# Optimization experiments

Measured on AMD Instinct MI355X. Metric: run time of the kernel, lower is better.

Reference implementation:

```python
import jax, jax.numpy as jnp
import numpy as np

B, T, C, H, W = 2, 4, 3, 96, 96
HF, L = 128, 6
TC = T * C
EPS = 1e-5


def swish(x):
    return x * jax.nn.sigmoid(x)


def _build_edges(h, w):
    # self-loops + 8-neighbor grid edges, exactly as image_to_graph
    edges = [np.stack([np.arange(h * w)] * 2)]
    nx0, ny0 = np.meshgrid(np.arange(w), np.arange(h), indexing='ij')
    for dx, dy in [(-1, -1), (0, -1), (1, -1), (-1, 0), (1, 0), (-1, 1), (0, 1), (1, 1)]:
        nx, ny = nx0 + dx, ny0 + dy
        src = ny * w + nx
        dst = (ny - dy) * w + (nx - dx)
        ok = (nx >= 0) & (nx < w) & (0 <= ny) & (ny < h)
        edges.append(np.stack([src[ok], dst[ok]]))
    return np.concatenate(edges, axis=1)


def setup_inputs() -> dict:
    key = jax.random.key(0)
    ks = iter(jax.random.split(key, 40))

    def lin(fi, fo):
        return jax.random.normal(next(ks), (fi, fo), jnp.float32) / np.sqrt(fi).astype(np.float32)

    x = jax.random.normal(next(ks), (B, T, C, H, W), jnp.float32)
    ei = _build_edges(H, W)
    px, py = np.meshgrid(np.arange(W), np.arange(H), indexing='ij')
    pos = np.stack([px.flatten(), py.flatten()], 1).astype(np.float32) / (H - 1)
    return dict(
        x=x,
        edge_src=jnp.asarray(ei[0], jnp.int32),
        edge_dst=jnp.asarray(ei[1], jnp.int32),
        pos=jnp.asarray(pos),
        emb_w1=lin(TC + 2, HF), emb_b1=jnp.zeros((HF,), jnp.float32),
        emb_w2=lin(HF, HF), emb_b2=jnp.zeros((HF,), jnp.float32),
        msg_w1=jnp.stack([lin(2 * HF + TC + 1, HF) for _ in range(L)]),
        msg_b1=jnp.zeros((L, HF), jnp.float32),
        msg_w2=jnp.stack([lin(HF, HF) for _ in range(L)]),
        msg_b2=jnp.zeros((L, HF), jnp.float32),
        upd_w1=jnp.stack([lin(2 * HF, HF) for _ in range(L)]),
        upd_b1=jnp.zeros((L, HF), jnp.float32),
        upd_w2=jnp.stack([lin(HF, HF) for _ in range(L)]),
        upd_b2=jnp.zeros((L, HF), jnp.float32),
        out_w1=lin(HF, HF), out_b1=jnp.zeros((HF,), jnp.float32),
        out_w2=lin(HF, C), out_b2=jnp.zeros((C,), jnp.float32),
    )


def _forward(x, emb_w1, emb_b1, emb_w2, emb_b2, msg_w1, msg_b1, msg_w2, msg_b2,
             upd_w1, upd_b1, upd_w2, upd_b2, out_w1, out_b1, out_w2, out_b2,
             edge_src, edge_dst, pos):
    b, t, c, h, w = x.shape
    n = h * w
    u = x.reshape(b, t * c, n).transpose(0, 2, 1)                       # [B,N,TC]
    node_in = jnp.concatenate([u, jnp.broadcast_to(pos, (b, n, 2))], -1)
    hf = swish(swish(node_in @ emb_w1 + emb_b1) @ emb_w2 + emb_b2)      # [B,N,HF]
    dist = jnp.linalg.norm(pos[edge_dst] - pos[edge_src], axis=1, keepdims=True)  # [E,1]
    dist_b = jnp.broadcast_to(dist, (b,) + dist.shape)
    deg = jnp.zeros((n,), x.dtype).at[edge_dst].add(1.0)                # >=1 (self loops)
    for l in range(msg_w1.shape[0]):
        m_in = jnp.concatenate([hf[:, edge_dst], hf[:, edge_src],
                                u[:, edge_dst] - u[:, edge_src], dist_b], -1)
        m = swish(swish(m_in @ msg_w1[l] + msg_b1[l]) @ msg_w2[l] + msg_b2[l])
        agg = jnp.zeros(hf.shape, hf.dtype).at[:, edge_dst].add(m) / deg[None, :, None]
        upd = swish(swish(jnp.concatenate([hf, agg], -1) @ upd_w1[l] + upd_b1[l])
                    @ upd_w2[l] + upd_b2[l])
        hf = hf + upd                                                    # residual (in==out)
        mu = hf.mean(axis=1, keepdims=True)                              # InstanceNorm per graph
        var = hf.var(axis=1, keepdims=True)
        hf = (hf - mu) * jax.lax.rsqrt(var + EPS)
    hg = hf.reshape(b, h, w, -1)
    diff = (swish(hg @ out_w1 + out_b1) @ out_w2 + out_b2).transpose(0, 3, 1, 2)
    return (x[:, -1] + diff)[:, None]                                    # [B,1,C,H,W]


def reference(x, edge_src, edge_dst, pos, emb_w1, emb_b1, emb_w2, emb_b2,
              msg_w1, msg_b1, msg_w2, msg_b2, upd_w1, upd_b1, upd_w2, upd_b2,
              out_w1, out_b1, out_w2, out_b2):
    return _forward(x, emb_w1, emb_b1, emb_w2, emb_b2, msg_w1, msg_b1, msg_w2, msg_b2,
                    upd_w1, upd_b1, upd_w2, upd_b2, out_w1, out_b1, out_w2, out_b2,
                    edge_src, edge_dst, pos)
```

## Files before the change

### kernel.cpp

```cpp
#include <hip/hip_runtime.h>
#include <math.h>

#define HF 128
#define NB 9216
#define BB 2
#define MROWS (BB*NB)
#define GH 96
#define GW 96
#define LAYERS 6

typedef __attribute__((ext_vector_type(8))) short bf16x8;
typedef __attribute__((ext_vector_type(4))) float f32x4;

#define MFMA16(a, b, c) __builtin_amdgcn_mfma_f32_16x16x32_bf16(a, b, c, 0, 0, 0)

__device__ __forceinline__ float swishf(float x) {
    return __fdividef(x, 1.0f + __expf(-x));
}

__device__ __forceinline__ unsigned short f2b(float f) {
    unsigned u = __float_as_uint(f);
    unsigned r = (u + 0x7fffu + ((u >> 16) & 1u)) >> 16;
    return (unsigned short)r;
}
__device__ __forceinline__ float b2f(unsigned short u) {
    return __uint_as_float((unsigned)u << 16);
}

__device__ __forceinline__ bf16x8 norm_frag(const float* __restrict__ hp,
                                            const float* __restrict__ mus,
                                            const float* __restrict__ rss, int k0) {
    float4 h0 = *(const float4*)hp;
    float4 h1 = *(const float4*)(hp + 4);
    float4 m0 = *(const float4*)&mus[k0];
    float4 m1 = *(const float4*)&mus[k0 + 4];
    float4 r0 = *(const float4*)&rss[k0];
    float4 r1 = *(const float4*)&rss[k0 + 4];
    union { bf16x8 v; unsigned u[4]; } az;
    float a0 = (h0.x - m0.x) * r0.x, a1 = (h0.y - m0.y) * r0.y;
    az.u[0] = (unsigned)f2b(a0) | ((unsigned)f2b(a1) << 16);
    float a2 = (h0.z - m0.z) * r0.z, a3 = (h0.w - m0.w) * r0.w;
    az.u[1] = (unsigned)f2b(a2) | ((unsigned)f2b(a3) << 16);
    float a4 = (h1.x - m1.x) * r1.x, a5 = (h1.y - m1.y) * r1.y;
    az.u[2] = (unsigned)f2b(a4) | ((unsigned)f2b(a5) << 16);
    float a6 = (h1.z - m1.z) * r1.z, a7 = (h1.w - m1.w) * r1.w;
    az.u[3] = (unsigned)f2b(a6) | ((unsigned)f2b(a7) << 16);
    return az.v;
}

__global__ void k_prep(const float* __restrict__ embw2, const float* __restrict__ outw1,
                       const float* __restrict__ msgw1, const float* __restrict__ msgw2,
                       const float* __restrict__ updw1, const float* __restrict__ updw2,
                       unsigned short* __restrict__ wT) {
    int s = blockIdx.x;
    const float* src;
    if (s == 0) src = embw2;
    else if (s == 1) src = outw1;
    else {
        int l = (s - 2) / 6, r = (s - 2) % 6;
        if (r == 0)      src = msgw1 + (size_t)l * 269 * HF;
        else if (r == 1) src = msgw1 + (size_t)l * 269 * HF + HF * HF;
        else if (r == 2) src = msgw2 + (size_t)l * HF * HF;
        else if (r == 3) src = updw1 + (size_t)l * 256 * HF;
        else if (r == 4) src = updw1 + (size_t)l * 256 * HF + HF * HF;
        else             src = updw2 + (size_t)l * HF * HF;
    }
    __shared__ float tile[128][133];
    int t = threadIdx.x;
#pragma unroll
    for (int i = 0; i < 64; ++i) {
        int id = i * 256 + t;
        tile[id >> 7][id & 127] = src[id];
    }
    __syncthreads();
    unsigned short* o = wT + (size_t)s * 16384;
#pragma unroll
    for (int i = 0; i < 64; ++i) {
        int id = i * 256 + t;
        int col = id >> 7, k = id & 127;
        o[id] = f2b(tile[k][col]);
    }
}

__global__ void k_build(const float* __restrict__ x, const float* __restrict__ pos,
                        float* __restrict__ nodein, float* __restrict__ musig) {
    int t = threadIdx.x;
    int idx = blockIdx.x * 256 + t;
    if (blockIdx.x == 0 && t < 256) {
        musig[t] = 0.0f;
        musig[256 + t] = 1.0f;
    }
    if (idx >= MROWS) return;
    int b = idx / NB, n = idx - b * NB;
    float* o = nodein + (size_t)idx * 16;
    const float* xb = x + (size_t)b * 12 * NB + n;
#pragma unroll
    for (int k = 0; k < 12; ++k) o[k] = xb[(size_t)k * NB];
    o[12] = pos[2 * n];
    o[13] = pos[2 * n + 1];
    o[14] = 0.0f; o[15] = 0.0f;
}

__global__ __launch_bounds__(256, 4)
void k_emb(const float* __restrict__ nodein, const float* __restrict__ w1,
           const float* __restrict__ b1, const unsigned short* __restrict__ wT2,
           const float* __restrict__ b2, float* __restrict__ hf) {
    __shared__ float xs[16][14];
    __shared__ char t1s[4096];
    int t = threadIdx.x;
    int rt = blockIdx.x * 16;
    if (t < 224) {
        int r = t / 14, k = t - r * 14;
        xs[r][k] = nodein[(size_t)(rt + r) * 16 + k];
    }
    __syncthreads();
    {
        int f = t & 127, rblk = t >> 7;
        float wreg[14];
#pragma unroll
        for (int k = 0; k < 14; ++k) wreg[k] = w1[k * HF + f];
        float bv = b1[f];
#pragma unroll
        for (int i = 0; i < 8; ++i) {
            int row = rblk * 8 + i;
            float acc = bv;
#pragma unroll
            for (int k = 0; k < 14; ++k) acc = fmaf(xs[row][k], wreg[k], acc);
            int addr = (row * 256 + f * 2) ^ ((row & 7) << 4);
            *(unsigned short*)(t1s + addr) = f2b(swishf(acc));
        }
    }
    __syncthreads();
    int wave = t >> 6, lane = t & 63, lr = lane & 15, lg = lane >> 4;
    int fb = wave * 32;
    f32x4 acc[2];
    acc[0] = (f32x4)0.0f; acc[1] = (f32x4)0.0f;
#pragma unroll
    for (int kc = 0; kc < 4; ++kc) {
        int k0 = kc * 32 + lg * 8;
        bf16x8 a = *(const bf16x8*)(t1s + ((lr * 256 + k0 * 2) ^ ((lr & 7) << 4)));
#pragma unroll
        for (int j = 0; j < 2; ++j) {
            bf16x8 b = *(const bf16x8*)(wT2 + (size_t)(fb + j * 16 + lr) * HF + k0);
            acc[j] = MFMA16(a, b, acc[j]);
        }
    }
#pragma unroll
    for (int j = 0; j < 2; ++j) {
        int f = fb + j * 16 + lr;
        float bv = b2[f];
#pragma unroll
        for (int r = 0; r < 4; ++r) {
            size_t o = (size_t)(rt + lg * 4 + r) * HF + f;
            hf[o] = swishf(acc[j][r] + bv);
        }
    }
}

__global__ __launch_bounds__(256, 4)
void k_as(const float* __restrict__ hf, const float* __restrict__ musig,
          const unsigned short* __restrict__ wA, const unsigned short* __restrict__ wB,
          const float* __restrict__ nodein, const float* __restrict__ w1u,
          unsigned short* __restrict__ A, unsigned short* __restrict__ S) {
    __shared__ float w1s[12][128];
    __shared__ float mus[128], rss[128];
    int t = threadIdx.x, wave = t >> 6, lane = t & 63, lr = lane & 15, lg = lane >> 4;
    int rt = blockIdx.x * 16;
    int b = blockIdx.x / (NB / 16);
    int fb = wave * 32;
    for (int i = t; i < 12 * 128; i += 256) w1s[i >> 7][i & 127] = w1u[i];
    if (t < 128) { mus[t] = musig[b * 128 + t]; rss[t] = musig[256 + b * 128 + t]; }
    __syncthreads();
    f32x4 accA[2], accS[2];
    accA[0] = (f32x4)0.0f; accA[1] = (f32x4)0.0f;
    accS[0] = (f32x4)0.0f; accS[1] = (f32x4)0.0f;
#pragma unroll
    for (int kc = 0; kc < 4; ++kc) {
        int k0 = kc * 32 + lg * 8;
        bf16x8 a = norm_frag(hf + (size_t)(rt + lr) * HF + k0, mus, rss, k0);
#pragma unroll
        for (int j = 0; j < 2; ++j) {
            bf16x8 bA = *(const bf16x8*)(wA + (size_t)(fb + j * 16 + lr) * HF + k0);
            accA[j] = MFMA16(a, bA, accA[j]);
            bf16x8 bS = *(const bf16x8*)(wB + (size_t)(fb + j * 16 + lr) * HF + k0);
            accS[j] = MFMA16(a, bS, accS[j]);
        }
    }
    float ni[4][12];
#pragma unroll
    for (int r = 0; r < 4; ++r) {
        const float4* np = (const float4*)(nodein + (size_t)(rt + lg * 4 + r) * 16);
        float4 v0 = np[0], v1 = np[1], v2 = np[2];
        ni[r][0] = v0.x; ni[r][1] = v0.y; ni[r][2] = v0.z; ni[r][3] = v0.w;
        ni[r][4] = v1.x; ni[r][5] = v1.y; ni[r][6] = v1.z; ni[r][7] = v1.w;
        ni[r][8] = v2.x; ni[r][9] = v2.y; ni[r][10] = v2.z; ni[r][11] = v2.w;
    }
#pragma unroll
    for (int j = 0; j < 2; ++j) {
        int f = fb + j * 16 + lr;
        float au[4] = {0.f, 0.f, 0.f, 0.f};
#pragma unroll
        for (int k = 0; k < 12; ++k) {
            float wv = w1s[k][f];
#pragma unroll
            for (int r = 0; r < 4; ++r) au[r] = fmaf(ni[r][k], wv, au[r]);
        }
#pragma unroll
        for (int r = 0; r < 4; ++r) {
            size_t o = (size_t)(rt + lg * 4 + r) * HF + f;
            A[o] = f2b(accA[j][r] + au[r]);
            S[o] = f2b(accS[j][r] - au[r]);
        }
    }
}

__global__ __launch_bounds__(256, 4)
void k_agg(const unsigned short* __restrict__ Ab, const unsigned short* __restrict__ Sb,
           const unsigned short* __restrict__ wT2, const float* __restrict__ b2,
           const float* __restrict__ b1, const float* __restrict__ w1d,
           unsigned short* __restrict__ aggb) {
    __shared__ float dsb[3][128];
    __shared__ char exb[9 * 4096];
    int t = threadIdx.x, kq = t >> 6, lane = t & 63, lr = lane & 15, lg = lane >> 4;
    int bx = blockIdx.x;
    int b = bx / (NB / 16), tile = bx % (NB / 16);
    int rt = tile * 16;
    int fb = kq * 32;
    size_t bN = (size_t)b * NB;
    int R = rt / GW, C0 = rt % GW;

    if (t < 128) {
        float bb = b1[t], wd = w1d[t];
        dsb[0][t] = bb;
        dsb[1][t] = fmaf(1.0f / 95.0f, wd, bb);
        dsb[2][t] = fmaf(1.4142135623730951f / 95.0f, wd, bb);
    }
    bf16x8 w2f[2][4];
#pragma unroll
    for (int j = 0; j < 2; ++j)
#pragma unroll
        for (int kc = 0; kc < 4; ++kc)
            w2f[j][kc] = *(const bf16x8*)(wT2 + (size_t)(fb + j * 16 + lr) * HF
                                          + kc * 32 + lg * 8);
    int rowA = rt + lr;
    float Af[8];
    {
        bf16x8 av = *(const bf16x8*)(Ab + (bN + rowA) * HF + kq * 32 + lg * 8);
#pragma unroll
        for (int e = 0; e < 8; ++e) Af[e] = b2f((unsigned short)av[e]);
    }
    float b2r[2] = { b2[fb + lr], b2[fb + 16 + lr] };
    int lofs = lane * 16;
    __syncthreads();

    bf16x8 sv;
    {
        int src = min(max(rowA - 97, 0), NB - 1);
        sv = *(const bf16x8*)(Sb + (bN + src) * HF + kq * 32 + lg * 8);
    }
#pragma unroll
    for (int off = 0; off < 9; ++off) {
        int dr = off / 3 - 1, dc = off % 3 - 1;
        int dd = dr * dr + dc * dc;
        bf16x8 cur = sv;
        if (off < 8) {
            int no = off + 1;
            int dnn = (no / 3 - 1) * GW + (no % 3 - 1);
            int src = min(max(rowA + dnn, 0), NB - 1);
            sv = *(const bf16x8*)(Sb + (bN + src) * HF + kq * 32 + lg * 8);
        }
        const float* dp = &dsb[dd][kq * 32 + lg * 8];
        union { bf16x8 v; unsigned u[4]; } az;
#pragma unroll
        for (int q = 0; q < 4; ++q) {
            float zl = swishf(Af[2 * q]     + b2f((unsigned short)cur[2 * q])     + dp[2 * q]);
            float zh = swishf(Af[2 * q + 1] + b2f((unsigned short)cur[2 * q + 1]) + dp[2 * q + 1]);
            az.u[q] = (unsigned)f2b(zl) | ((unsigned)f2b(zh) << 16);
        }
        *(bf16x8*)(exb + off * 4096 + kq * 1024 + lofs) = az.v;
    }
    __syncthreads();

    f32x4 agg2[2];
    agg2[0] = (f32x4)0.0f; agg2[1] = (f32x4)0.0f;
#pragma unroll
    for (int off = 0; off < 9; ++off) {
        int dr = off / 3 - 1, dc = off % 3 - 1;
        f32x4 acc[2];
        acc[0] = (f32x4)0.0f; acc[1] = (f32x4)0.0f;
#pragma unroll
        for (int kc = 0; kc < 4; ++kc) {
            bf16x8 a = *(const bf16x8*)(exb + off * 4096 + kc * 1024 + lofs);
            acc[0] = MFMA16(a, w2f[0][kc], acc[0]);
            acc[1] = MFMA16(a, w2f[1][kc], acc[1]);
        }
        bool rOK = (unsigned)(R + dr) < (unsigned)GH;
#pragma unroll
        for (int j = 0; j < 2; ++j)
#pragma unroll
            for (int r = 0; r < 4; ++r) {
                int C = C0 + lg * 4 + r;
                if (rOK && (unsigned)(C + dc) < (unsigned)GW)
                    agg2[j][r] += swishf(acc[j][r] + b2r[j]);
            }
    }
    float nr = 1.0f + (R > 0) + (R < GH - 1);
#pragma unroll
    for (int j = 0; j < 2; ++j)
#pragma unroll
        for (int r = 0; r < 4; ++r) {
            int n = rt + lg * 4 + r;
            int C = C0 + lg * 4 + r;
            float nc = 1.0f + (C > 0) + (C < GW - 1);
            aggb[(bN + n) * HF + fb + j * 16 + lr] =
                f2b(__fdividef(agg2[j][r], nr * nc));
        }
}

__global__ __launch_bounds__(256, 4)
void k_upd(float* __restrict__ hf, const float* __restrict__ musig,
           const unsigned short* __restrict__ aggb,
           const unsigned short* __restrict__ w1a, const unsigned short* __restrict__ w1b,
           const unsigned short* __restrict__ w2, const float* __restrict__ b1v,
           const float* __restrict__ b2v, float* __restrict__ partial) {
    __shared__ char t1s[4096];
    __shared__ float mus[128], rss[128];
    int t = threadIdx.x, wave = t >> 6, lane = t & 63, lr = lane & 15, lg = lane >> 4;
    int rt = blockIdx.x * 16;
    int b = blockIdx.x / (NB / 16);
    int fb = wave * 32;
    if (t < 128) { mus[t] = musig[b * 128 + t]; rss[t] = musig[256 + b * 128 + t]; }
    __syncthreads();
    f32x4 acc[2];
    acc[0] = (f32x4)0.0f; acc[1] = (f32x4)0.0f;
#pragma unroll
    for (int kc = 0; kc < 4; ++kc) {
        int k0 = kc * 32 + lg * 8;
        bf16x8 a1 = norm_frag(hf + (size_t)(rt + lr) * HF + k0, mus, rss, k0);
        bf16x8 a2 = *(const bf16x8*)(aggb + (size_t)(rt + lr) * HF + k0);
#pragma unroll
        for (int j = 0; j < 2; ++j) {
            bf16x8 bA = *(const bf16x8*)(w1a + (size_t)(fb + j * 16 + lr) * HF + k0);
            acc[j] = MFMA16(a1, bA, acc[j]);
            bf16x8 bB = *(const bf16x8*)(w1b + (size_t)(fb + j * 16 + lr) * HF + k0);
            acc[j] = MFMA16(a2, bB, acc[j]);
        }
    }
#pragma unroll
    for (int j = 0; j < 2; ++j) {
        int col = fb + j * 16 + lr;
        float bv = b1v[col];
#pragma unroll
        for (int r = 0; r < 4; ++r) {
            int row = lg * 4 + r;
            int addr = (row * 256 + col * 2) ^ ((row & 7) << 4);
            *(unsigned short*)(t1s + addr) = f2b(swishf(acc[j][r] + bv));
        }
    }
    __syncthreads();
    f32x4 acc2[2];
    acc2[0] = (f32x4)0.0f; acc2[1] = (f32x4)0.0f;
#pragma unroll
    for (int kc = 0; kc < 4; ++kc) {
        int k0 = kc * 32 + lg * 8;
        bf16x8 a = *(const bf16x8*)(t1s + ((lr * 256 + k0 * 2) ^ ((lr & 7) << 4)));
#pragma unroll
        for (int j = 0; j < 2; ++j) {
            bf16x8 b = *(const bf16x8*)(w2 + (size_t)(fb + j * 16 + lr) * HF + k0);
            acc2[j] = MFMA16(a, b, acc2[j]);
        }
    }
#pragma unroll
    for (int j = 0; j < 2; ++j) {
        int f = fb + j * 16 + lr;
        float bv = b2v[f];
        float mu = mus[f], rs = rss[f];
        float s1 = 0.f, s2 = 0.f;
#pragma unroll
        for (int r = 0; r < 4; ++r) {
            size_t o = (size_t)(rt + lg * 4 + r) * HF + f;
            float v = swishf(acc2[j][r] + bv) + (hf[o] - mu) * rs;
            hf[o] = v;
            s1 += v; s2 += v * v;
        }
        s1 += __shfl_xor(s1, 16); s1 += __shfl_xor(s1, 32);
        s2 += __shfl_xor(s2, 16); s2 += __shfl_xor(s2, 32);
        if (lg == 0) {
            float* p = partial + ((size_t)blockIdx.x * HF + f) * 2;
            p[0] = s1; p[1] = s2;
        }
    }
}

__global__ void k_stats(const float* __restrict__ partial, float* __restrict__ musig) {
    __shared__ float ss[256], qq[256];
    int bx = blockIdx.x;
    int b = bx >> 7, f = bx & 127;
    int t = threadIdx.x;
    float s = 0.f, q = 0.f;
    for (int i = t; i < 576; i += 256) {
        const float* p = partial + (((size_t)(b * 576 + i)) * HF + f) * 2;
        s += p[0]; q += p[1];
    }
    ss[t] = s; qq[t] = q;
    __syncthreads();
    for (int st = 128; st > 0; st >>= 1) {
        if (t < st) { ss[t] += ss[t + st]; qq[t] += qq[t + st]; }
        __syncthreads();
    }
    if (t == 0) {
        float mu = ss[0] * (1.0f / NB);
        float var = qq[0] * (1.0f / NB) - mu * mu;
        musig[bx] = mu;
        musig[256 + bx] = rsqrtf(var + 1e-5f);
    }
}

__global__ __launch_bounds__(256, 4)
void k_out(const float* __restrict__ hf, const float* __restrict__ musig,
           const unsigned short* __restrict__ wT1, const float* __restrict__ b1,
           const float* __restrict__ w2, const float* __restrict__ b2,
           const float* __restrict__ x, float* __restrict__ out) {
    __shared__ float g1s[16][132];
    __shared__ float w2s[384];
    __shared__ float mus[128], rss[128];
    int t = threadIdx.x, wave = t >> 6, lane = t & 63, lr = lane & 15, lg = lane >> 4;
    int rt = blockIdx.x * 16;
    int b = blockIdx.x / (NB / 16);
    int fb = wave * 32;
    for (int i = t; i < 384; i += 256) w2s[i] = w2[i];
    if (t < 128) { mus[t] = musig[b * 128 + t]; rss[t] = musig[256 + b * 128 + t]; }
    __syncthreads();
    f32x4 acc[2];
    acc[0] = (f32x4)0.0f; acc[1] = (f32x4)0.0f;
#pragma unroll
    for (int kc = 0; kc < 4; ++kc) {
        int k0 = kc * 32 + lg * 8;
        bf16x8 a = norm_frag(hf + (size_t)(rt + lr) * HF + k0, mus, rss, k0);
#pragma unroll
        for (int j = 0; j < 2; ++j) {
            bf16x8 bfr = *(const bf16x8*)(wT1 + (size_t)(fb + j * 16 + lr) * HF + k0);
            acc[j] = MFMA16(a, bfr, acc[j]);
        }
    }
#pragma unroll
    for (int j = 0; j < 2; ++j) {
        int f = fb + j * 16 + lr;
        float bv = b1[f];
#pragma unroll
        for (int r = 0; r < 4; ++r)
            g1s[lg * 4 + r][f] = swishf(acc[j][r] + bv);
    }
    __syncthreads();
    if (t < 48) {
        int r = t / 3, c = t - (t / 3) * 3;
        int row = rt + r;
        int bb = row / NB, n = row - bb * NB;
        float a = b2[c];
#pragma unroll 8
        for (int k = 0; k < HF; ++k) a = fmaf(g1s[r][k], w2s[k * 3 + c], a);
        float xv = x[(((size_t)bb * 4 + 3) * 3 + c) * NB + n];
        out[((size_t)bb * 3 + c) * NB + n] = a + xv;
    }
}

extern "C" void kernel_launch(void* const* d_in, const int* in_sizes, int n_in,
                              void* d_out, int out_size, void* d_ws, size_t ws_size,
                              hipStream_t stream) {
    const float* x      = (const float*)d_in[0];
    const float* pos    = (const float*)d_in[3];
    const float* emb_w1 = (const float*)d_in[4];
    const float* emb_b1 = (const float*)d_in[5];
    const float* emb_b2 = (const float*)d_in[7];
    const float* msg_w1 = (const float*)d_in[8];
    const float* msg_b1 = (const float*)d_in[9];
    const float* msg_b2 = (const float*)d_in[11];
    const float* upd_b1 = (const float*)d_in[13];
    const float* upd_b2 = (const float*)d_in[15];
    const float* out_b1 = (const float*)d_in[17];
    const float* out_w2 = (const float*)d_in[18];
    const float* out_b2 = (const float*)d_in[19];

    float* w = (float*)d_ws;
    size_t off = 0;
    auto alloc = [&](size_t n) { float* p = w + off; off += n; return p; };
    float* nodein  = alloc((size_t)MROWS * 16);
    float* hf      = alloc((size_t)MROWS * HF);
    float* partial = alloc((size_t)1152 * HF * 2);
    float* musig   = alloc(512);
    unsigned short* aggb = (unsigned short*)alloc((size_t)MROWS * 64);
    unsigned short* Abf  = (unsigned short*)alloc((size_t)MROWS * 64);
    unsigned short* Sbf  = (unsigned short*)alloc((size_t)MROWS * 64);
    unsigned short* wT   = (unsigned short*)alloc((size_t)38 * 16384 / 2);
    (void)ws_size; (void)in_sizes; (void)n_in; (void)out_size;

    k_prep<<<38, 256, 0, stream>>>((const float*)d_in[6], (const float*)d_in[16],
                                   msg_w1, (const float*)d_in[10],
                                   (const float*)d_in[12], (const float*)d_in[14], wT);
    k_build<<<(MROWS + 255) / 256, 256, 0, stream>>>(x, pos, nodein, musig);
    k_emb<<<1152, 256, 0, stream>>>(nodein, emb_w1, emb_b1, wT + 0 * 16384, emb_b2, hf);
    for (int l = 0; l < LAYERS; ++l) {
        const unsigned short* wL = wT + (size_t)(2 + 6 * l) * 16384;
        const float* W1 = msg_w1 + (size_t)l * 269 * HF;
        k_as<<<1152, 256, 0, stream>>>(hf, musig, wL + 0 * 16384, wL + 1 * 16384,
                                       nodein, W1 + 256 * HF, Abf, Sbf);
        k_agg<<<1152, 256, 0, stream>>>(Abf, Sbf, wL + 2 * 16384, msg_b2 + l * HF,
                                        msg_b1 + l * HF, W1 + 268 * HF, aggb);
        k_upd<<<1152, 256, 0, stream>>>(hf, musig, aggb, wL + 3 * 16384, wL + 4 * 16384,
                                        wL + 5 * 16384, upd_b1 + l * HF,
                                        upd_b2 + l * HF, partial);
        k_stats<<<256, 256, 0, stream>>>(partial, musig);
    }
    k_out<<<1152, 256, 0, stream>>>(hf, musig, wT + 1 * 16384, out_b1, out_w2, out_b2,
                                    x, (float*)d_out);
}
```

Before: 522.8 us.

## Fuse aggregation with update kernel and replace stats pass with atomics

Merges the message aggregation kernel and the node update kernel into one, so the aggregated features stay in shared memory as bf16 and are not written to and re-read from global memory. The separate statistics reduction kernel is removed. Per-block feature sums and sums of squares are now atomically added into a per-layer buffer, and each consumer derives mean and rsqrt variance when it loads them. This cuts two launches and one global round-trip per layer. In exchange it adds atomic contention on 512 floats and makes the float summation order nondeterministic.

Measured after the change: 459.6 us. -12.1%, faster.

```diff
diff --git a/kernel.cpp b/kernel.cpp
--- a/kernel.cpp
+++ b/kernel.cpp
@@ -48,6 +48,20 @@
     return az.v;
 }
 
+__device__ __forceinline__ void load_musig(const float* __restrict__ mraw, int b, int t,
+                                           float* __restrict__ mus, float* __restrict__ rss) {
+    if (t < 128) {
+        float mu = 0.f, rs = 1.f;
+        if (mraw) {
+            float s = mraw[b * 128 + t], q = mraw[256 + b * 128 + t];
+            mu = s * (1.0f / NB);
+            float var = q * (1.0f / NB) - mu * mu;
+            rs = rsqrtf(var + 1e-5f);
+        }
+        mus[t] = mu; rss[t] = rs;
+    }
+}
+
 __global__ void k_prep(const float* __restrict__ embw2, const float* __restrict__ outw1,
                        const float* __restrict__ msgw1, const float* __restrict__ msgw2,
                        const float* __restrict__ updw1, const float* __restrict__ updw2,
@@ -83,13 +97,9 @@
 }
 
 __global__ void k_build(const float* __restrict__ x, const float* __restrict__ pos,
-                        float* __restrict__ nodein, float* __restrict__ musig) {
-    int t = threadIdx.x;
-    int idx = blockIdx.x * 256 + t;
-    if (blockIdx.x == 0 && t < 256) {
-        musig[t] = 0.0f;
-        musig[256 + t] = 1.0f;
-    }
+                        float* __restrict__ nodein, float* __restrict__ msr) {
+    int idx = blockIdx.x * 256 + threadIdx.x;
+    if (idx < LAYERS * 512) msr[idx] = 0.0f;
     if (idx >= MROWS) return;
     int b = idx / NB, n = idx - b * NB;
     float* o = nodein + (size_t)idx * 16;
@@ -158,7 +168,7 @@
 }
 
 __global__ __launch_bounds__(256, 4)
-void k_as(const float* __restrict__ hf, const float* __restrict__ musig,
+void k_as(const float* __restrict__ hf, const float* __restrict__ mraw,
           const unsigned short* __restrict__ wA, const unsigned short* __restrict__ wB,
           const float* __restrict__ nodein, const float* __restrict__ w1u,
           unsigned short* __restrict__ A, unsigned short* __restrict__ S) {
@@ -169,7 +179,7 @@
     int b = blockIdx.x / (NB / 16);
     int fb = wave * 32;
     for (int i = t; i < 12 * 128; i += 256) w1s[i >> 7][i & 127] = w1u[i];
-    if (t < 128) { mus[t] = musig[b * 128 + t]; rss[t] = musig[256 + b * 128 + t]; }
+    load_musig(mraw, b, t, mus, rss);
     __syncthreads();
     f32x4 accA[2], accS[2];
     accA[0] = (f32x4)0.0f; accA[1] = (f32x4)0.0f;
@@ -215,11 +225,15 @@
 }
 
 __global__ __launch_bounds__(256, 4)
-void k_agg(const unsigned short* __restrict__ Ab, const unsigned short* __restrict__ Sb,
-           const unsigned short* __restrict__ wT2, const float* __restrict__ b2,
-           const float* __restrict__ b1, const float* __restrict__ w1d,
-           unsigned short* __restrict__ aggb) {
+void k_aggupd(const unsigned short* __restrict__ Ab, const unsigned short* __restrict__ Sb,
+              const unsigned short* __restrict__ wT2, const float* __restrict__ b2m,
+              const float* __restrict__ b1m, const float* __restrict__ w1d,
+              float* __restrict__ hf, const float* __restrict__ mraw,
+              const unsigned short* __restrict__ w1a, const unsigned short* __restrict__ w1b,
+              const unsigned short* __restrict__ w2u, const float* __restrict__ b1u,
+              const float* __restrict__ b2u, float* __restrict__ msr) {
     __shared__ float dsb[3][128];
+    __shared__ float mus[128], rss[128];
     __shared__ char exb[9 * 4096];
     int t = threadIdx.x, kq = t >> 6, lane = t & 63, lr = lane & 15, lg = lane >> 4;
     int bx = blockIdx.x;
@@ -230,11 +244,12 @@
     int R = rt / GW, C0 = rt % GW;
 
     if (t < 128) {
-        float bb = b1[t], wd = w1d[t];
+        float bb = b1m[t], wd = w1d[t];
         dsb[0][t] = bb;
         dsb[1][t] = fmaf(1.0f / 95.0f, wd, bb);
         dsb[2][t] = fmaf(1.4142135623730951f / 95.0f, wd, bb);
     }
+    load_musig(mraw, b, t, mus, rss);
     bf16x8 w2f[2][4];
 #pragma unroll
     for (int j = 0; j < 2; ++j)
@@ -249,7 +264,7 @@
 #pragma unroll
         for (int e = 0; e < 8; ++e) Af[e] = b2f((unsigned short)av[e]);
     }
-    float b2r[2] = { b2[fb + lr], b2[fb + 16 + lr] };
+    float b2r[2] = { b2m[fb + lr], b2m[fb + 16 + lr] };
     int lofs = lane * 16;
     __syncthreads();
 
@@ -304,40 +319,29 @@
                     agg2[j][r] += swishf(acc[j][r] + b2r[j]);
             }
     }
+    __syncthreads();
+
     float nr = 1.0f + (R > 0) + (R < GH - 1);
 #pragma unroll
     for (int j = 0; j < 2; ++j)
 #pragma unroll
         for (int r = 0; r < 4; ++r) {
-            int n = rt + lg * 4 + r;
-            int C = C0 + lg * 4 + r;
+            int row = lg * 4 + r;
+            int C = C0 + row;
             float nc = 1.0f + (C > 0) + (C < GW - 1);
-            aggb[(bN + n) * HF + fb + j * 16 + lr] =
-                f2b(__fdividef(agg2[j][r], nr * nc));
-        }
-}
-
-__global__ __launch_bounds__(256, 4)
-void k_upd(float* __restrict__ hf, const float* __restrict__ musig,
-           const unsigned short* __restrict__ aggb,
-           const unsigned short* __restrict__ w1a, const unsigned short* __restrict__ w1b,
-           const unsigned short* __restrict__ w2, const float* __restrict__ b1v,
-           const float* __restrict__ b2v, float* __restrict__ partial) {
-    __shared__ char t1s[4096];
-    __shared__ float mus[128], rss[128];
-    int t = threadIdx.x, wave = t >> 6, lane = t & 63, lr = lane & 15, lg = lane >> 4;
-    int rt = blockIdx.x * 16;
-    int b = blockIdx.x / (NB / 16);
-    int fb = wave * 32;
-    if (t < 128) { mus[t] = musig[b * 128 + t]; rss[t] = musig[256 + b * 128 + t]; }
-    __syncthreads();
+            int f = fb + j * 16 + lr;
+            int addr = (row * 256 + f * 2) ^ ((row & 7) << 4);
+            *(unsigned short*)(exb + addr) = f2b(__fdividef(agg2[j][r], nr * nc));
+        }
+    __syncthreads();
+
     f32x4 acc[2];
     acc[0] = (f32x4)0.0f; acc[1] = (f32x4)0.0f;
 #pragma unroll
     for (int kc = 0; kc < 4; ++kc) {
         int k0 = kc * 32 + lg * 8;
-        bf16x8 a1 = norm_frag(hf + (size_t)(rt + lr) * HF + k0, mus, rss, k0);
-        bf16x8 a2 = *(const bf16x8*)(aggb + (size_t)(rt + lr) * HF + k0);
+        bf16x8 a1 = norm_frag(hf + (bN + rt + lr) * HF + k0, mus, rss, k0);
+        bf16x8 a2 = *(const bf16x8*)(exb + ((lr * 256 + k0 * 2) ^ ((lr & 7) << 4)));
 #pragma unroll
         for (int j = 0; j < 2; ++j) {
             bf16x8 bA = *(const bf16x8*)(w1a + (size_t)(fb + j * 16 + lr) * HF + k0);
@@ -349,12 +353,12 @@
 #pragma unroll
     for (int j = 0; j < 2; ++j) {
         int col = fb + j * 16 + lr;
-        float bv = b1v[col];
+        float bv = b1u[col];
 #pragma unroll
         for (int r = 0; r < 4; ++r) {
             int row = lg * 4 + r;
             int addr = (row * 256 + col * 2) ^ ((row & 7) << 4);
-            *(unsigned short*)(t1s + addr) = f2b(swishf(acc[j][r] + bv));
+            *(unsigned short*)(exb + 4096 + addr) = f2b(swishf(acc[j][r] + bv));
         }
     }
     __syncthreads();
@@ -363,22 +367,22 @@
 #pragma unroll
     for (int kc = 0; kc < 4; ++kc) {
         int k0 = kc * 32 + lg * 8;
-        bf16x8 a = *(const bf16x8*)(t1s + ((lr * 256 + k0 * 2) ^ ((lr & 7) << 4)));
+        bf16x8 a = *(const bf16x8*)(exb + 4096 + ((lr * 256 + k0 * 2) ^ ((lr & 7) << 4)));
 #pragma unroll
         for (int j = 0; j < 2; ++j) {
-            bf16x8 b = *(const bf16x8*)(w2 + (size_t)(fb + j * 16 + lr) * HF + k0);
-            acc2[j] = MFMA16(a, b, acc2[j]);
+            bf16x8 bfr = *(const bf16x8*)(w2u + (size_t)(fb + j * 16 + lr) * HF + k0);
+            acc2[j] = MFMA16(a, bfr, acc2[j]);
         }
     }
 #pragma unroll
     for (int j = 0; j < 2; ++j) {
         int f = fb + j * 16 + lr;
-        float bv = b2v[f];
+        float bv = b2u[f];
         float mu = mus[f], rs = rss[f];
         float s1 = 0.f, s2 = 0.f;
 #pragma unroll
         for (int r = 0; r < 4; ++r) {
-            size_t o = (size_t)(rt + lg * 4 + r) * HF + f;
+            size_t o = (bN + rt + lg * 4 + r) * HF + f;
             float v = swishf(acc2[j][r] + bv) + (hf[o] - mu) * rs;
             hf[o] = v;
             s1 += v; s2 += v * v;
@@ -386,38 +390,14 @@
         s1 += __shfl_xor(s1, 16); s1 += __shfl_xor(s1, 32);
         s2 += __shfl_xor(s2, 16); s2 += __shfl_xor(s2, 32);
         if (lg == 0) {
-            float* p = partial + ((size_t)blockIdx.x * HF + f) * 2;
-            p[0] = s1; p[1] = s2;
-        }
-    }
-}
-
-__global__ void k_stats(const float* __restrict__ partial, float* __restrict__ musig) {
-    __shared__ float ss[256], qq[256];
-    int bx = blockIdx.x;
-    int b = bx >> 7, f = bx & 127;
-    int t = threadIdx.x;
-    float s = 0.f, q = 0.f;
-    for (int i = t; i < 576; i += 256) {
-        const float* p = partial + (((size_t)(b * 576 + i)) * HF + f) * 2;
-        s += p[0]; q += p[1];
-    }
-    ss[t] = s; qq[t] = q;
-    __syncthreads();
-    for (int st = 128; st > 0; st >>= 1) {
-        if (t < st) { ss[t] += ss[t + st]; qq[t] += qq[t + st]; }
-        __syncthreads();
-    }
-    if (t == 0) {
-        float mu = ss[0] * (1.0f / NB);
-        float var = qq[0] * (1.0f / NB) - mu * mu;
-        musig[bx] = mu;
-        musig[256 + bx] = rsqrtf(var + 1e-5f);
+            atomicAdd(&msr[b * 128 + f], s1);
+            atomicAdd(&msr[256 + b * 128 + f], s2);
+        }
     }
 }
 
 __global__ __launch_bounds__(256, 4)
-void k_out(const float* __restrict__ hf, const float* __restrict__ musig,
+void k_out(const float* __restrict__ hf, const float* __restrict__ mraw,
            const unsigned short* __restrict__ wT1, const float* __restrict__ b1,
            const float* __restrict__ w2, const float* __restrict__ b2,
            const float* __restrict__ x, float* __restrict__ out) {
@@ -429,7 +409,7 @@
     int b = blockIdx.x / (NB / 16);
     int fb = wave * 32;
     for (int i = t; i < 384; i += 256) w2s[i] = w2[i];
-    if (t < 128) { mus[t] = musig[b * 128 + t]; rss[t] = musig[256 + b * 128 + t]; }
+    load_musig(mraw, b, t, mus, rss);
     __syncthreads();
     f32x4 acc[2];
     acc[0] = (f32x4)0.0f; acc[1] = (f32x4)0.0f;
@@ -486,9 +466,7 @@
     auto alloc = [&](size_t n) { float* p = w + off; off += n; return p; };
     float* nodein  = alloc((size_t)MROWS * 16);
     float* hf      = alloc((size_t)MROWS * HF);
-    float* partial = alloc((size_t)1152 * HF * 2);
-    float* musig   = alloc(512);
-    unsigned short* aggb = (unsigned short*)alloc((size_t)MROWS * 64);
+    float* msr     = alloc((size_t)LAYERS * 512);
     unsigned short* Abf  = (unsigned short*)alloc((size_t)MROWS * 64);
     unsigned short* Sbf  = (unsigned short*)alloc((size_t)MROWS * 64);
     unsigned short* wT   = (unsigned short*)alloc((size_t)38 * 16384 / 2);
@@ -497,20 +475,22 @@
     k_prep<<<38, 256, 0, stream>>>((const float*)d_in[6], (const float*)d_in[16],
                                    msg_w1, (const float*)d_in[10],
                                    (const float*)d_in[12], (const float*)d_in[14], wT);
-    k_build<<<(MROWS + 255) / 256, 256, 0, stream>>>(x, pos, nodein, musig);
+    k_build<<<(MROWS + 255) / 256, 256, 0, stream>>>(x, pos, nodein, msr);
     k_emb<<<1152, 256, 0, stream>>>(nodein, emb_w1, emb_b1, wT + 0 * 16384, emb_b2, hf);
     for (int l = 0; l < LAYERS; ++l) {
         const unsigned short* wL = wT + (size_t)(2 + 6 * l) * 16384;
         const float* W1 = msg_w1 + (size_t)l * 269 * HF;
-        k_as<<<1152, 256, 0, stream>>>(hf, musig, wL + 0 * 16384, wL + 1 * 16384,
+        const float* mprev = (l == 0) ? nullptr : msr + (size_t)(l - 1) * 512;
+        k_as<<<1152, 256, 0, stream>>>(hf, mprev, wL + 0 * 16384, wL + 1 * 16384,
                                        nodein, W1 + 256 * HF, Abf, Sbf);
-        k_agg<<<1152, 256, 0, stream>>>(Abf, Sbf, wL + 2 * 16384, msg_b2 + l * HF,
-                                        msg_b1 + l * HF, W1 + 268 * HF, aggb);
-        k_upd<<<1152, 256, 0, stream>>>(hf, musig, aggb, wL + 3 * 16384, wL + 4 * 16384,
-                                        wL + 5 * 16384, upd_b1 + l * HF,
-                                        upd_b2 + l * HF, partial);
-        k_stats<<<256, 256, 0, stream>>>(partial, musig);
-    }
-    k_out<<<1152, 256, 0, stream>>>(hf, musig, wT + 1 * 16384, out_b1, out_w2, out_b2,
+        k_aggupd<<<1152, 256, 0, stream>>>(Abf, Sbf, wL + 2 * 16384, msg_b2 + l * HF,
+                                           msg_b1 + l * HF, W1 + 268 * HF,
+                                           hf, mprev,
+                                           wL + 3 * 16384, wL + 4 * 16384,
+                                           wL + 5 * 16384, upd_b1 + l * HF,
+                                           upd_b2 + l * HF, msr + (size_t)l * 512);
+    }
+    k_out<<<1152, 256, 0, stream>>>(hf, msr + (size_t)(LAYERS - 1) * 512,
+                                    wT + 1 * 16384, out_b1, out_w2, out_b2,
                                     x, (float*)d_out);
 }
```
